# Performance work log

Hardware: AMD Instinct MI355X
Metric: run time of the kernel (lower is better)

The kernel has to match this reference:

```python
import jax, jax.numpy as jnp
import numpy as np

COPIES = 4
OUT_BITS = 8
N = 2 ** OUT_BITS
IN_DIMS = 1024
BATCH = 256
CHANS = 2 * COPIES + 1  # skip=True


def setup_inputs() -> dict:
    key = jax.random.key(0)
    k1, k2 = jax.random.split(key)
    inp = jax.random.normal(k1, (BATCH, IN_DIMS), dtype=jnp.float32)
    # xavier-uniform-ish linear weight, zero bias
    fan = IN_DIMS + CHANS * N
    lim = np.sqrt(6.0 / fan)
    W_xy = jax.random.uniform(k2, (CHANS * N, IN_DIMS), dtype=jnp.float32, minval=-lim, maxval=lim)
    b_xy = jnp.zeros((CHANS * N,), dtype=jnp.float32)
    # Conv1d(copies+1, 1, 1) initialized to constant 1/(2*copies+1), zero bias
    w_out = jnp.full((COPIES + 1,), 1.0 / CHANS, dtype=jnp.float32)
    b_out = jnp.zeros((1,), dtype=jnp.float32)
    return {"input": inp, "W_xy": W_xy, "b_xy": b_xy, "w_out": w_out, "b_out": b_out}


def _soft_xor(x, y):
    # x, y: [M, N]; z[m, j] = logsumexp_i (x[m, i] + y[m, i ^ j])
    idx = jnp.arange(N)[:, None] ^ jnp.arange(N)[None, :]  # [N, N]
    return jax.nn.logsumexp(x[:, :, None] + y[:, idx], axis=1)  # [M, N]


def reference(input, W_xy, b_xy, w_out, b_out):
    B = input.shape[0]
    xy = input @ W_xy.T + b_xy                      # [B, CHANS*N]
    x = xy[:, : COPIES * N].reshape(B * COPIES, N)
    y = xy[:, COPIES * N : 2 * COPIES * N].reshape(B * COPIES, N)
    skip = xy[:, 2 * COPIES * N :].reshape(B, 1, N)
    z = _soft_xor(x, y).reshape(B, COPIES, N)
    z = jnp.concatenate([z, skip], axis=1)          # [B, COPIES+1, N]
    out = jnp.einsum("bcn,c->bn", z, w_out) + b_out  # 1x1 conv -> squeeze
    return out
```

## Files before the change

kernel.cpp:

```cpp
#include <hip/hip_runtime.h>
#include <hip/hip_bf16.h>

#define K_DIM   1024
#define N_OUT   256
#define XY_COLS 2304

typedef __bf16 bf16x4 __attribute__((ext_vector_type(4)));
typedef __bf16 bf16x8 __attribute__((ext_vector_type(8)));
typedef float  f32x4  __attribute__((ext_vector_type(4)));

__global__ __launch_bounds__(256) void gemm_xy_kernel(
    const float* __restrict__ A,
    const float* __restrict__ W,
    const float* __restrict__ bias,
    float* __restrict__ xy)
{
    const int t   = threadIdx.x;
    const int bid = blockIdx.x;
    const int mt  = bid / 36;
    const int nt  = bid - mt * 36;
    const int m0  = mt * 32;
    const int n0  = nt * 64;

    __shared__ __align__(16) __bf16 sA[32][32];
    __shared__ __align__(16) __bf16 sB[64][32];

    const int ra = t >> 3;
    const int ka = (t & 7) * 4;
    const int rw = t >> 2;
    const int kw = (t & 3) * 8;

    const float* pA = A + (m0 + ra) * K_DIM + ka;
    const float* pW = W + (n0 + rw) * K_DIM + kw;

    const int lane = t & 63;
    const int wv   = t >> 6;
    const int mh   = wv >> 1;
    const int nh   = wv & 1;
    const int l15  = lane & 15;
    const int quad = lane >> 4;

    f32x4 acc0 = {0.f, 0.f, 0.f, 0.f};
    f32x4 acc1 = {0.f, 0.f, 0.f, 0.f};

    float4 ar  = *(const float4*)pA;
    float4 wr0 = *(const float4*)pW;
    float4 wr1 = *(const float4*)(pW + 4);

    #pragma unroll 1
    for (int kk = 0; kk < K_DIM / 32; ++kk) {
        if (kk) __syncthreads();
        bf16x4 av = { (__bf16)ar.x, (__bf16)ar.y, (__bf16)ar.z, (__bf16)ar.w };
        *(bf16x4*)&sA[ra][ka] = av;
        bf16x8 wvec = { (__bf16)wr0.x, (__bf16)wr0.y, (__bf16)wr0.z, (__bf16)wr0.w,
                        (__bf16)wr1.x, (__bf16)wr1.y, (__bf16)wr1.z, (__bf16)wr1.w };
        *(bf16x8*)&sB[rw][kw] = wvec;
        if (kk + 1 < K_DIM / 32) {
            pA += 32; pW += 32;
            ar  = *(const float4*)pA;
            wr0 = *(const float4*)pW;
            wr1 = *(const float4*)(pW + 4);
        }
        __syncthreads();
        bf16x8 af  = *(bf16x8*)&sA[16 * mh + l15][quad * 8];
        bf16x8 bf0 = *(bf16x8*)&sB[32 * nh + l15][quad * 8];
        bf16x8 bf1 = *(bf16x8*)&sB[32 * nh + 16 + l15][quad * 8];
        acc0 = __builtin_amdgcn_mfma_f32_16x16x32_bf16(af, bf0, acc0, 0, 0, 0);
        acc1 = __builtin_amdgcn_mfma_f32_16x16x32_bf16(af, bf1, acc1, 0, 0, 0);
    }

    const int row0 = m0 + 16 * mh + quad * 4;
    const int col0 = n0 + 32 * nh + l15;
    const float b0 = bias[col0];
    const float b1 = bias[col0 + 16];
    #pragma unroll
    for (int r = 0; r < 4; ++r) {
        xy[(row0 + r) * XY_COLS + col0]      = acc0[r] + b0;
        xy[(row0 + r) * XY_COLS + col0 + 16] = acc1[r] + b1;
    }
}

__global__ __launch_bounds__(512) void softxor_kernel(
    const float* __restrict__ xy,
    const float* __restrict__ w_out,
    const float* __restrict__ b_out,
    float* __restrict__ out)
{
    const int b = blockIdx.x;
    const int t = threadIdx.x;

    __shared__ __align__(16) float ex[4][N_OUT];
    __shared__ __align__(16) float ey[4][N_OUT];
    __shared__ __align__(16) float sk[N_OUT];
    __shared__ __align__(16) float part[8][N_OUT];

    const float* row = xy + (long)b * XY_COLS;

    for (int e4 = t; e4 < XY_COLS / 4; e4 += 512) {
        float4 v = *(const float4*)(row + e4 * 4);
        int e = e4 * 4;
        if (e < 1024) {
            float* d = &ex[e >> 8][e & 255];
            d[0] = __expf(v.x); d[1] = __expf(v.y); d[2] = __expf(v.z); d[3] = __expf(v.w);
        } else if (e < 2048) {
            float* d = &ey[(e >> 8) - 4][e & 255];
            d[0] = __expf(v.x); d[1] = __expf(v.y); d[2] = __expf(v.z); d[3] = __expf(v.w);
        } else {
            float* d = &sk[e - 2048];
            d[0] = v.x; d[1] = v.y; d[2] = v.z; d[3] = v.w;
        }
    }
    __syncthreads();

    const int wv = t >> 6;
    const int c  = wv >> 1;
    const int h  = wv & 1;
    const int jh = t & 63;

    float S0 = 0.f, S1 = 0.f, S2 = 0.f, S3 = 0.f;
    const int ih0 = h * 32;
    #pragma unroll 4
    for (int ih = ih0; ih < ih0 + 32; ++ih) {
        float4 xa = *(const float4*)&ex[c][ih * 4];
        float4 yb = *(const float4*)&ey[c][(ih ^ jh) * 4];
        S0 += xa.x * yb.x + xa.y * yb.y + xa.z * yb.z + xa.w * yb.w;
        S1 += xa.x * yb.y + xa.y * yb.x + xa.z * yb.w + xa.w * yb.z;
        S2 += xa.x * yb.z + xa.y * yb.w + xa.z * yb.x + xa.w * yb.y;
        S3 += xa.x * yb.w + xa.y * yb.z + xa.z * yb.y + xa.w * yb.x;
    }
    *(float4*)&part[wv][jh * 4] = make_float4(S0, S1, S2, S3);
    __syncthreads();

    if (t < N_OUT) {
        float acc = w_out[4] * sk[t] + b_out[0];
        #pragma unroll
        for (int cc = 0; cc < 4; ++cc) {
            float S = part[2 * cc][t] + part[2 * cc + 1][t];
            acc += w_out[cc] * __logf(S);
        }
        out[b * N_OUT + t] = acc;
    }
}

extern "C" void kernel_launch(void* const* d_in, const int* in_sizes, int n_in,
                              void* d_out, int out_size, void* d_ws, size_t ws_size,
                              hipStream_t stream) {
    const float* input = (const float*)d_in[0];
    const float* W_xy  = (const float*)d_in[1];
    const float* b_xy  = (const float*)d_in[2];
    const float* w_out = (const float*)d_in[3];
    const float* b_out = (const float*)d_in[4];
    float* outp = (float*)d_out;
    float* xy   = (float*)d_ws;

    gemm_xy_kernel<<<288, 256, 0, stream>>>(input, W_xy, b_xy, xy);
    softxor_kernel<<<256, 512, 0, stream>>>(xy, w_out, b_out, outp);
}
```

Before: 92.16 us.

## Split GEMM K across waves and load MFMA fragments directly from global

The GEMM block tile changes from 32x64 to 64x32. Each of the four waves now owns one quarter of the K dimension and loads its bf16 MFMA fragments straight from global memory into registers, with no per-step shared-memory staging or barriers. Partial accumulators are summed across the waves through shared memory at the end before the bias is added and results are stored. This removes the 32 barrier-separated iterations and gives each wave more MFMAs per load, at the cost of a larger register footprint, uncoalesced strided global fragment loads, and a final shared-memory reduction.

After: 94.62 us. +2.7%, slower.

```diff
diff --git a/kernel.cpp b/kernel.cpp
--- a/kernel.cpp
+++ b/kernel.cpp
@@ -5,9 +5,14 @@
 #define N_OUT   256
 #define XY_COLS 2304
 
-typedef __bf16 bf16x4 __attribute__((ext_vector_type(4)));
 typedef __bf16 bf16x8 __attribute__((ext_vector_type(8)));
 typedef float  f32x4  __attribute__((ext_vector_type(4)));
+
+static __device__ __forceinline__ bf16x8 cvt8(float4 lo, float4 hi) {
+    bf16x8 r = { (__bf16)lo.x, (__bf16)lo.y, (__bf16)lo.z, (__bf16)lo.w,
+                 (__bf16)hi.x, (__bf16)hi.y, (__bf16)hi.z, (__bf16)hi.w };
+    return r;
+}
 
 __global__ __launch_bounds__(256) void gemm_xy_kernel(
     const float* __restrict__ A,
@@ -15,68 +20,78 @@
     const float* __restrict__ bias,
     float* __restrict__ xy)
 {
-    const int t   = threadIdx.x;
-    const int bid = blockIdx.x;
-    const int mt  = bid / 36;
-    const int nt  = bid - mt * 36;
-    const int m0  = mt * 32;
-    const int n0  = nt * 64;
-
-    __shared__ __align__(16) __bf16 sA[32][32];
-    __shared__ __align__(16) __bf16 sB[64][32];
-
-    const int ra = t >> 3;
-    const int ka = (t & 7) * 4;
-    const int rw = t >> 2;
-    const int kw = (t & 3) * 8;
-
-    const float* pA = A + (m0 + ra) * K_DIM + ka;
-    const float* pW = W + (n0 + rw) * K_DIM + kw;
-
+    const int t    = threadIdx.x;
     const int lane = t & 63;
-    const int wv   = t >> 6;
-    const int mh   = wv >> 1;
-    const int nh   = wv & 1;
+    const int w    = t >> 6;
+    const int bid  = blockIdx.x;
+    const int m    = bid / 72;
+    const int n    = bid - m * 72;
     const int l15  = lane & 15;
     const int quad = lane >> 4;
 
-    f32x4 acc0 = {0.f, 0.f, 0.f, 0.f};
-    f32x4 acc1 = {0.f, 0.f, 0.f, 0.f};
+    const int m0 = m * 64;
+    const int n0 = n * 32;
 
-    float4 ar  = *(const float4*)pA;
-    float4 wr0 = *(const float4*)pW;
-    float4 wr1 = *(const float4*)(pW + 4);
+    const float* pa[4];
+    #pragma unroll
+    for (int mi = 0; mi < 4; ++mi)
+        pa[mi] = A + (size_t)(m0 + mi * 16 + l15) * K_DIM + w * 256 + quad * 8;
+    const float* pb[2];
+    #pragma unroll
+    for (int nj = 0; nj < 2; ++nj)
+        pb[nj] = W + (size_t)(n0 + nj * 16 + l15) * K_DIM + w * 256 + quad * 8;
+
+    f32x4 acc[8];
+    #pragma unroll
+    for (int i = 0; i < 8; ++i) acc[i] = (f32x4){0.f, 0.f, 0.f, 0.f};
+
+    float4 a0[4], a1[4], b0[2], b1[2];
+    #pragma unroll
+    for (int mi = 0; mi < 4; ++mi) { a0[mi] = *(const float4*)pa[mi]; a1[mi] = *(const float4*)(pa[mi] + 4); }
+    #pragma unroll
+    for (int nj = 0; nj < 2; ++nj) { b0[nj] = *(const float4*)pb[nj]; b1[nj] = *(const float4*)(pb[nj] + 4); }
 
     #pragma unroll 1
-    for (int kk = 0; kk < K_DIM / 32; ++kk) {
-        if (kk) __syncthreads();
-        bf16x4 av = { (__bf16)ar.x, (__bf16)ar.y, (__bf16)ar.z, (__bf16)ar.w };
-        *(bf16x4*)&sA[ra][ka] = av;
-        bf16x8 wvec = { (__bf16)wr0.x, (__bf16)wr0.y, (__bf16)wr0.z, (__bf16)wr0.w,
-                        (__bf16)wr1.x, (__bf16)wr1.y, (__bf16)wr1.z, (__bf16)wr1.w };
-        *(bf16x8*)&sB[rw][kw] = wvec;
-        if (kk + 1 < K_DIM / 32) {
-            pA += 32; pW += 32;
-            ar  = *(const float4*)pA;
-            wr0 = *(const float4*)pW;
-            wr1 = *(const float4*)(pW + 4);
+    for (int s = 0; s < 8; ++s) {
+        bf16x8 av[4], bv[2];
+        #pragma unroll
+        for (int mi = 0; mi < 4; ++mi) av[mi] = cvt8(a0[mi], a1[mi]);
+        #pragma unroll
+        for (int nj = 0; nj < 2; ++nj) bv[nj] = cvt8(b0[nj], b1[nj]);
+
+        if (s < 7) {
+            const int ko = (s + 1) * 32;
+            #pragma unroll
+            for (int mi = 0; mi < 4; ++mi) { a0[mi] = *(const float4*)(pa[mi] + ko); a1[mi] = *(const float4*)(pa[mi] + ko + 4); }
+            #pragma unroll
+            for (int nj = 0; nj < 2; ++nj) { b0[nj] = *(const float4*)(pb[nj] + ko); b1[nj] = *(const float4*)(pb[nj] + ko + 4); }
         }
-        __syncthreads();
-        bf16x8 af  = *(bf16x8*)&sA[16 * mh + l15][quad * 8];
-        bf16x8 bf0 = *(bf16x8*)&sB[32 * nh + l15][quad * 8];
-        bf16x8 bf1 = *(bf16x8*)&sB[32 * nh + 16 + l15][quad * 8];
-        acc0 = __builtin_amdgcn_mfma_f32_16x16x32_bf16(af, bf0, acc0, 0, 0, 0);
-        acc1 = __builtin_amdgcn_mfma_f32_16x16x32_bf16(af, bf1, acc1, 0, 0, 0);
+
+        #pragma unroll
+        for (int mi = 0; mi < 4; ++mi)
+            #pragma unroll
+            for (int nj = 0; nj < 2; ++nj)
+                acc[mi * 2 + nj] = __builtin_amdgcn_mfma_f32_16x16x32_bf16(av[mi], bv[nj], acc[mi * 2 + nj], 0, 0, 0);
     }
 
-    const int row0 = m0 + 16 * mh + quad * 4;
-    const int col0 = n0 + 32 * nh + l15;
-    const float b0 = bias[col0];
-    const float b1 = bias[col0 + 16];
+    __shared__ __align__(16) f32x4 red[4][8][64];
     #pragma unroll
-    for (int r = 0; r < 4; ++r) {
-        xy[(row0 + r) * XY_COLS + col0]      = acc0[r] + b0;
-        xy[(row0 + r) * XY_COLS + col0 + 16] = acc1[r] + b1;
+    for (int i = 0; i < 8; ++i) red[w][i][lane] = acc[i];
+    __syncthreads();
+
+    #pragma unroll
+    for (int idx = t; idx < 512; idx += 256) {
+        const int tile = idx >> 6;
+        const int l    = idx & 63;
+        f32x4 s = red[0][tile][l] + red[1][tile][l] + red[2][tile][l] + red[3][tile][l];
+        const int mi  = tile >> 1;
+        const int nj  = tile & 1;
+        const int row = m0 + mi * 16 + (l >> 4) * 4;
+        const int col = n0 + nj * 16 + (l & 15);
+        const float bcol = bias[col];
+        #pragma unroll
+        for (int r = 0; r < 4; ++r)
+            xy[(size_t)(row + r) * XY_COLS + col] = s[r] + bcol;
     }
 }
 
```
